# Optimization experiments

Hardware: AMD Instinct MI355X
Metric: run time of the kernel (lower is better)

## Reference

```python
import jax, jax.numpy as jnp
import numpy as np

B, S, D, H, F = 64, 512, 1024, 1024, 1024  # note: module requires H == D
EPS = 1e-6


def setup_inputs() -> dict:
    key = jax.random.key(0)
    ks = jax.random.split(key, 14)
    p = lambda k, shape: 0.02 * jax.random.normal(k, shape, dtype=jnp.float32)
    return {
        "hidden_state": jax.random.normal(ks[0], (B, S, D), dtype=jnp.float32),
        "field_hidden_state": jax.random.normal(ks[1], (B, S, F), dtype=jnp.float32),
        "input": jax.random.normal(ks[2], (B, D), dtype=jnp.float32),
        "finished": jnp.zeros((B, 1), dtype=bool),
        "W1": p(ks[3], (H, D)), "b1": p(ks[4], (H,)),
        "W2": p(ks[5], (H, D)), "b2": p(ks[6], (H,)),
        "W3": p(ks[7], (H, 2 * D)), "b3": p(ks[8], (H,)),
        "W4": p(ks[9], (H, F)), "b4": p(ks[10], (H,)),
        "W5": p(ks[11], (H, D)), "b5": p(ks[12], (H,)),
    }


def _norm_over_seq(w):
    # manual exp/max/sum softmax over seq dim (axis 0) with 1e-6 guard, as in torch
    w = jnp.exp(w - jnp.max(w, axis=0, keepdims=True))
    return w / (EPS + jnp.sum(w, axis=0, keepdims=True))


def reference(hidden_state, field_hidden_state, input, finished,
              W1, b1, W2, b2, W3, b3, W4, b4, W5, b5):
    hs = jnp.transpose(hidden_state, (1, 0, 2))        # [S, B, D]
    fs = jnp.transpose(field_hidden_state, (1, 0, 2))  # [S, B, F]
    phi_h = jnp.tanh(hs @ W1.T + b1)                   # [S, B, H]
    phi_f = jnp.tanh(fs @ W4.T + b4)                   # [S, B, H]

    gamma_h = jnp.tanh(input @ W2.T + b2)              # [B, H]
    weights = _norm_over_seq(jnp.sum(phi_h * gamma_h, axis=2, keepdims=True))  # [S, B, 1]

    alpha_h = jnp.tanh(input @ W5.T + b5)              # [B, H]
    field_w = _norm_over_seq(jnp.sum(phi_f * alpha_h, axis=2, keepdims=True))  # [S, B, 1]

    wf = weights * field_w
    weights = wf / (EPS + jnp.sum(wf, axis=0, keepdims=True))  # [S, B, 1]

    context = jnp.sum(hs * weights, axis=0)            # [B, D]
    out = jnp.concatenate([context, input], axis=-1) @ W3.T + b3  # [B, H]
    out = jnp.where(finished, jnp.zeros_like(out), out)
    return out, weights
```

## Files before the change

kernel.cpp:

```cpp
#include <hip/hip_runtime.h>

#define EPS 1e-6f

typedef _Float16 f16;
typedef __fp16 h16x2 __attribute__((ext_vector_type(2)));
typedef _Float16 f16x4 __attribute__((ext_vector_type(4)));
typedef _Float16 f16x8 __attribute__((ext_vector_type(8)));
typedef float f32x4 __attribute__((ext_vector_type(4)));

__device__ __forceinline__ float tanh_fast(float x) {
    float e = __expf(2.0f * x);
    return 1.0f - 2.0f / (e + 1.0f);
}

__global__ __launch_bounds__(256) void wconv_kernel(
    const float* __restrict__ W1, const float* __restrict__ W4,
    f16* __restrict__ W1h, f16* __restrict__ W4h)
{
    int gid = blockIdx.x * 256 + threadIdx.x;
    const float4* s1 = (const float4*)W1;
    const float4* s4 = (const float4*)W4;
    f16x4* d1 = (f16x4*)W1h;
    f16x4* d4 = (f16x4*)W4h;
    #pragma unroll
    for (int r = 0; r < 2; ++r) {
        int i = gid + r * 131072;
        float4 v = s1[i];
        f16x4 o; o[0]=(f16)v.x; o[1]=(f16)v.y; o[2]=(f16)v.z; o[3]=(f16)v.w;
        d1[i] = o;
        float4 u = s4[i];
        f16x4 p; p[0]=(f16)u.x; p[1]=(f16)u.y; p[2]=(f16)u.z; p[3]=(f16)u.w;
        d4[i] = p;
    }
}

__global__ __launch_bounds__(256) void gamal_kernel(
    const float* __restrict__ inp,
    const float* __restrict__ W2, const float* __restrict__ b2,
    const float* __restrict__ W5, const float* __restrict__ b5,
    float* __restrict__ gamm, float* __restrict__ alph)
{
    const float* W  = blockIdx.y ? W5 : W2;
    const float* bs = blockIdx.y ? b5 : b2;
    float* dst      = blockIdx.y ? alph : gamm;
    int wid = threadIdx.x >> 6, lane = threadIdx.x & 63;
    int p = blockIdx.x * 4 + wid;
    int b = p >> 10, h = p & 1023;
    const float4* wr = (const float4*)(W + (size_t)h * 1024);
    const float4* xr = (const float4*)(inp + (size_t)b * 1024);
    float acc = 0.f;
    #pragma unroll
    for (int j = 0; j < 4; ++j) {
        float4 w4 = wr[lane + 64 * j];
        float4 x4 = xr[lane + 64 * j];
        acc += w4.x * x4.x + w4.y * x4.y + w4.z * x4.z + w4.w * x4.w;
    }
    #pragma unroll
    for (int o = 32; o; o >>= 1) acc += __shfl_xor(acc, o);
    if (lane == 0) dst[p] = tanh_fast(acc + bs[h]);
}

__global__ __launch_bounds__(512, 1) void gemm_logits_kernel(
    const float* __restrict__ Ahid, const float* __restrict__ Afld,
    const f16* __restrict__ W1h, const f16* __restrict__ W4h,
    const float* __restrict__ b1, const float* __restrict__ b4,
    const float* __restrict__ gamm, const float* __restrict__ alph,
    float* __restrict__ Lpart)
{
    __shared__ __align__(16) char smA[2][32768];
    __shared__ __align__(16) char smW[2][32768];
    __shared__ float rowpart[256][4];

    const int lin = blockIdx.x;
    const int swz = (lin & 7) * 128 + (lin >> 3);
    const int mat = swz >> 9;
    const int rem = swz & 511;
    const int m_blk = rem >> 2;
    const int nc = rem & 3;
    const int m0 = m_blk << 8;
    const int hc0 = nc << 8;

    const float* A  = mat ? Afld : Ahid;
    const f16*  W   = mat ? W4h : W1h;
    const float* bv = mat ? b4 : b1;
    const float* gv = mat ? alph : gamm;

    const int t = threadIdx.x;
    const int lane = t & 63;
    const int wv = t >> 6;
    const int wr = wv >> 2;
    const int wc = wv & 3;
    const int c16 = lane & 15;
    const int kg = lane >> 4;

    const int srow = t >> 1;
    const int shalf = t & 1;
    const float* aRow = A + (size_t)(m0 + srow) * 1024 + shalf * 32;

    const int lrow = lane >> 3, lslot = lane & 7;
    const int kchunk = lslot ^ lrow;

    const int swzr = (c16 & 7) << 4;
    const int aoffb = (wr * 128 + c16) * 128;
    const int woffb = (wc * 64 + c16) * 128;
    const int kg16 = kg * 16;

    f32x4 acc[8][4];
    #pragma unroll
    for (int i = 0; i < 8; ++i)
        #pragma unroll
        for (int j = 0; j < 4; ++j) acc[i][j] = (f32x4){0.f, 0.f, 0.f, 0.f};

    float4 a_ld[8];

    auto loadA = [&](int kt) {
        const float4* ap = (const float4*)(aRow + kt * 64);
        #pragma unroll
        for (int j = 0; j < 8; ++j) a_ld[j] = ap[j];
    };
    auto writeA = [&](char* buf) {
        char* ad = buf + srow * 128;
        const int swzw = (srow & 7) << 4;
        const int wb = shalf * 64;
        #pragma unroll
        for (int j = 0; j < 4; ++j) {
            union { f16x8 v; h16x2 h[4]; } u;
            float4 x = a_ld[2 * j], y = a_ld[2 * j + 1];
            u.h[0] = __builtin_amdgcn_cvt_pkrtz(x.x, x.y);
            u.h[1] = __builtin_amdgcn_cvt_pkrtz(x.z, x.w);
            u.h[2] = __builtin_amdgcn_cvt_pkrtz(y.x, y.y);
            u.h[3] = __builtin_amdgcn_cvt_pkrtz(y.z, y.w);
            *(f16x8*)(ad + ((wb + j * 16) ^ swzw)) = u.v;
        }
    };
    auto gloadW = [&](int kt, char* buf) {
        #pragma unroll
        for (int j = 0; j < 4; ++j) {
            int r = wv * 32 + j * 8;
            const f16* src = W + (size_t)(hc0 + r + lrow) * 1024 + kt * 64 + kchunk * 8;
            char* dst = buf + r * 128;
            __builtin_amdgcn_global_load_lds(
                (const __attribute__((address_space(1))) void*)src,
                (__attribute__((address_space(3))) void*)dst, 16, 0, 0);
        }
    };

    loadA(0);
    gloadW(0, smW[0]);
    writeA(smA[0]);
    loadA(1);
    asm volatile("s_waitcnt vmcnt(8) lgkmcnt(0)" ::: "memory");
    __builtin_amdgcn_sched_barrier(0);
    __builtin_amdgcn_s_barrier();
    __builtin_amdgcn_sched_barrier(0);

    int cur = 0;
    for (int kt = 0; kt < 16; ++kt) {
        const int ktn  = kt < 15 ? kt + 1 : 15;
        const int ktnn = kt < 14 ? kt + 2 : 15;
        char* aC = smA[cur];
        char* wC = smW[cur];
        char* aN = smA[cur ^ 1];
        char* wN = smW[cur ^ 1];

        gloadW(ktn, wN);

        {
            f16x8 af[8], wf[4];
            const int ko = kg16 ^ swzr;
            #pragma unroll
            for (int mi = 0; mi < 8; ++mi) af[mi] = *(const f16x8*)(aC + aoffb + mi * 2048 + ko);
            #pragma unroll
            for (int ni = 0; ni < 4; ++ni) wf[ni] = *(const f16x8*)(wC + woffb + ni * 2048 + ko);
            __builtin_amdgcn_s_setprio(1);
            #pragma unroll
            for (int ni = 0; ni < 4; ++ni)
                #pragma unroll
                for (int mi = 0; mi < 8; ++mi)
                    acc[mi][ni] = __builtin_amdgcn_mfma_f32_16x16x32_f16(af[mi], wf[ni], acc[mi][ni], 0, 0, 0);
            __builtin_amdgcn_s_setprio(0);
        }

        writeA(aN);
        loadA(ktnn);
        __builtin_amdgcn_sched_barrier(0);

        {
            f16x8 af[8], wf[4];
            const int ko = (64 + kg16) ^ swzr;
            #pragma unroll
            for (int mi = 0; mi < 8; ++mi) af[mi] = *(const f16x8*)(aC + aoffb + mi * 2048 + ko);
            #pragma unroll
            for (int ni = 0; ni < 4; ++ni) wf[ni] = *(const f16x8*)(wC + woffb + ni * 2048 + ko);
            __builtin_amdgcn_s_setprio(1);
            #pragma unroll
            for (int ni = 0; ni < 4; ++ni)
                #pragma unroll
                for (int mi = 0; mi < 8; ++mi)
                    acc[mi][ni] = __builtin_amdgcn_mfma_f32_16x16x32_f16(af[mi], wf[ni], acc[mi][ni], 0, 0, 0);
            __builtin_amdgcn_s_setprio(0);
        }

        asm volatile("s_waitcnt vmcnt(8) lgkmcnt(0)" ::: "memory");
        __builtin_amdgcn_sched_barrier(0);
        __builtin_amdgcn_s_barrier();
        __builtin_amdgcn_sched_barrier(0);
        cur ^= 1;
    }

    const int bidx = m_blk >> 1;
    float g[4], bb[4];
    #pragma unroll
    for (int ni = 0; ni < 4; ++ni) {
        int h = hc0 + wc * 64 + ni * 16 + c16;
        g[ni]  = gv[(bidx << 10) + h];
        bb[ni] = bv[h];
    }
    #pragma unroll
    for (int mi = 0; mi < 8; ++mi) {
        #pragma unroll
        for (int q = 0; q < 4; ++q) {
            float v = tanh_fast(acc[mi][0][q] + bb[0]) * g[0]
                    + tanh_fast(acc[mi][1][q] + bb[1]) * g[1]
                    + tanh_fast(acc[mi][2][q] + bb[2]) * g[2]
                    + tanh_fast(acc[mi][3][q] + bb[3]) * g[3];
            v += __shfl_xor(v, 1);
            v += __shfl_xor(v, 2);
            v += __shfl_xor(v, 4);
            v += __shfl_xor(v, 8);
            if (c16 == 0)
                rowpart[wr * 128 + mi * 16 + kg * 4 + q][wc] = v;
        }
    }
    __syncthreads();
    if (t < 256)
        Lpart[(size_t)(mat * 4 + nc) * 32768 + m0 + t] =
            rowpart[t][0] + rowpart[t][1] + rowpart[t][2] + rowpart[t][3];
}

__device__ __forceinline__ float blockMax(float v, float* sm) {
    #pragma unroll
    for (int o = 32; o; o >>= 1) v = fmaxf(v, __shfl_xor(v, o));
    if ((threadIdx.x & 63) == 0) sm[threadIdx.x >> 6] = v;
    __syncthreads();
    v = fmaxf(fmaxf(sm[0], sm[1]), fmaxf(sm[2], sm[3]));
    __syncthreads();
    return v;
}
__device__ __forceinline__ float blockSum(float v, float* sm) {
    #pragma unroll
    for (int o = 32; o; o >>= 1) v += __shfl_xor(v, o);
    if ((threadIdx.x & 63) == 0) sm[threadIdx.x >> 6] = v;
    __syncthreads();
    v = sm[0] + sm[1] + sm[2] + sm[3];
    __syncthreads();
    return v;
}

__global__ __launch_bounds__(256) void softmax_combine_kernel(
    const float* __restrict__ Lp,
    float* __restrict__ wfin, float* __restrict__ dout)
{
    __shared__ float sm[4];
    int b = blockIdx.x, t = threadIdx.x;
    float h0 = 0.f, h1 = 0.f, f0 = 0.f, f1 = 0.f;
    #pragma unroll
    for (int nc = 0; nc < 4; ++nc) {
        h0 += Lp[nc * 32768 + b * 512 + t];
        h1 += Lp[nc * 32768 + b * 512 + 256 + t];
        f0 += Lp[(4 + nc) * 32768 + b * 512 + t];
        f1 += Lp[(4 + nc) * 32768 + b * 512 + 256 + t];
    }
    float mh = blockMax(fmaxf(h0, h1), sm);
    float mf = blockMax(fmaxf(f0, f1), sm);
    float e0 = __expf(h0 - mh), e1 = __expf(h1 - mh);
    float q0 = __expf(f0 - mf), q1 = __expf(f1 - mf);
    float sh = blockSum(e0 + e1, sm);
    float sf = blockSum(q0 + q1, sm);
    float wh0 = e0 / (EPS + sh), wh1 = e1 / (EPS + sh);
    float wq0 = q0 / (EPS + sf), wq1 = q1 / (EPS + sf);
    float c0 = wh0 * wq0, c1 = wh1 * wq1;
    float sc = blockSum(c0 + c1, sm);
    float r0 = c0 / (EPS + sc), r1 = c1 / (EPS + sc);
    wfin[b * 512 + t]       = r0;
    wfin[b * 512 + 256 + t] = r1;
    dout[65536 + t * 64 + b]         = r0;
    dout[65536 + (256 + t) * 64 + b] = r1;
}

__global__ __launch_bounds__(256) void context_kernel(
    const float* __restrict__ hs, const float* __restrict__ wgt,
    float* __restrict__ ctxpart)
{
    int dq = blockIdx.x;
    int b  = blockIdx.y;
    int sh = blockIdx.z;
    int t = threadIdx.x;
    int ss = t >> 6, ds = t & 63;
    __shared__ float4 part[4][64];
    const float4* hp = (const float4*)hs;
    float ax = 0.f, ay = 0.f, az = 0.f, aw = 0.f;
    int sBase = sh * 256 + ss * 64;
    for (int i = 0; i < 64; ++i) {
        int s = sBase + i;
        float w = wgt[b * 512 + s];
        float4 v = hp[(size_t)(b * 512 + s) * 256 + dq * 64 + ds];
        ax += v.x * w; ay += v.y * w; az += v.z * w; aw += v.w * w;
    }
    float4 r; r.x = ax; r.y = ay; r.z = az; r.w = aw;
    part[ss][ds] = r;
    __syncthreads();
    if (ss == 0) {
        float4 a0 = part[0][ds], a1 = part[1][ds], a2 = part[2][ds], a3 = part[3][ds];
        float4 o;
        o.x = a0.x + a1.x + a2.x + a3.x;
        o.y = a0.y + a1.y + a2.y + a3.y;
        o.z = a0.z + a1.z + a2.z + a3.z;
        o.w = a0.w + a1.w + a2.w + a3.w;
        ((float4*)ctxpart)[(size_t)sh * 16384 + b * 256 + dq * 64 + ds] = o;
    }
}

__global__ __launch_bounds__(256) void out_kernel(
    const float* __restrict__ ctxpart, const float* __restrict__ inp,
    const float* __restrict__ W3, const float* __restrict__ b3,
    const unsigned char* __restrict__ fin, float* __restrict__ out)
{
    int t = threadIdx.x, wid = t >> 6, lane = t & 63;
    int h = blockIdx.x * 4 + wid;
    __shared__ __align__(16) float xs[2048];
    float4* xsv = (float4*)xs;
    float4 wreg[8];
    const float4* w3r = (const float4*)(W3 + (size_t)h * 2048);
    #pragma unroll
    for (int j = 0; j < 8; ++j) wreg[j] = w3r[lane + 64 * j];
    const float4* cp = (const float4*)ctxpart;
    const float4* xp = (const float4*)inp;
    for (int b = 0; b < 64; ++b) {
        __syncthreads();
        {
            float4 c0 = cp[b * 256 + t];
            float4 c1 = cp[16384 + b * 256 + t];
            float4 cc; cc.x = c0.x + c1.x; cc.y = c0.y + c1.y;
            cc.z = c0.z + c1.z; cc.w = c0.w + c1.w;
            xsv[t] = cc;
            xsv[256 + t] = xp[b * 256 + t];
        }
        __syncthreads();
        float acc = 0.f;
        #pragma unroll
        for (int j = 0; j < 8; ++j) {
            float4 x = xsv[lane + 64 * j];
            acc += wreg[j].x * x.x + wreg[j].y * x.y + wreg[j].z * x.z + wreg[j].w * x.w;
        }
        #pragma unroll
        for (int o = 32; o; o >>= 1) acc += __shfl_xor(acc, o);
        if (lane == 0) out[b * 1024 + h] = fin[b] ? 0.f : (acc + b3[h]);
    }
}

extern "C" void kernel_launch(void* const* d_in, const int* in_sizes, int n_in,
                              void* d_out, int out_size, void* d_ws, size_t ws_size,
                              hipStream_t stream)
{
    const float* hidden = (const float*)d_in[0];
    const float* field  = (const float*)d_in[1];
    const float* input  = (const float*)d_in[2];
    const unsigned char* fin = (const unsigned char*)d_in[3];
    const float* W1 = (const float*)d_in[4];
    const float* b1 = (const float*)d_in[5];
    const float* W2 = (const float*)d_in[6];
    const float* b2 = (const float*)d_in[7];
    const float* W3 = (const float*)d_in[8];
    const float* b3 = (const float*)d_in[9];
    const float* W4 = (const float*)d_in[10];
    const float* b4 = (const float*)d_in[11];
    const float* W5 = (const float*)d_in[12];
    const float* b5 = (const float*)d_in[13];
    float* out = (float*)d_out;

    char* ws = (char*)d_ws;
    float* Lpart = (float*)(ws);
    float* wfin  = (float*)(ws + 1048576);
    float* gamm  = (float*)(ws + 1179648);
    float* alph  = (float*)(ws + 1441792);
    float* ctxp  = (float*)(ws + 1703936);
    f16*   W1h   = (f16*)(ws + 2228224);
    f16*   W4h   = (f16*)(ws + 4325376);

    wconv_kernel<<<512, 256, 0, stream>>>(W1, W4, W1h, W4h);
    gamal_kernel<<<dim3(16384, 2), 256, 0, stream>>>(input, W2, b2, W5, b5, gamm, alph);
    gemm_logits_kernel<<<1024, 512, 0, stream>>>(hidden, field, W1h, W4h,
                                                 b1, b4, gamm, alph, Lpart);
    softmax_combine_kernel<<<64, 256, 0, stream>>>(Lpart, wfin, out);
    context_kernel<<<dim3(4, 64, 2), 256, 0, stream>>>(hidden, wfin, ctxp);
    out_kernel<<<256, 256, 0, stream>>>(ctxp, input, W3, b3, fin, out);
}
```

Measured before the change: 379.4 us.

## Split GEMM k-step into four interleaved phases with staggered loads and barriers

Restructures the main GEMM loop so each k-tile is computed in four smaller MFMA clusters of 4x4 tiles instead of two 8x4 clusters. The W global-to-LDS loads and the A conversion writes are split into halves and interleaved between the clusters, with extra workgroup barriers intended to keep waves in lockstep so memory and matrix work overlap. This lowers register pressure for fragments but adds many more barriers and lgkmcnt waits per iteration, which can serialize the waves.

```diff
diff --git a/kernel.cpp b/kernel.cpp
--- a/kernel.cpp
+++ b/kernel.cpp
@@ -118,24 +118,24 @@
         #pragma unroll
         for (int j = 0; j < 8; ++j) a_ld[j] = ap[j];
     };
-    auto writeA = [&](char* buf) {
+    auto writeA_half = [&](char* buf, int h) {
         char* ad = buf + srow * 128;
         const int swzw = (srow & 7) << 4;
         const int wb = shalf * 64;
         #pragma unroll
-        for (int j = 0; j < 4; ++j) {
-            union { f16x8 v; h16x2 h[4]; } u;
+        for (int j = 2 * h; j < 2 * h + 2; ++j) {
+            union { f16x8 v; h16x2 q[4]; } u;
             float4 x = a_ld[2 * j], y = a_ld[2 * j + 1];
-            u.h[0] = __builtin_amdgcn_cvt_pkrtz(x.x, x.y);
-            u.h[1] = __builtin_amdgcn_cvt_pkrtz(x.z, x.w);
-            u.h[2] = __builtin_amdgcn_cvt_pkrtz(y.x, y.y);
-            u.h[3] = __builtin_amdgcn_cvt_pkrtz(y.z, y.w);
+            u.q[0] = __builtin_amdgcn_cvt_pkrtz(x.x, x.y);
+            u.q[1] = __builtin_amdgcn_cvt_pkrtz(x.z, x.w);
+            u.q[2] = __builtin_amdgcn_cvt_pkrtz(y.x, y.y);
+            u.q[3] = __builtin_amdgcn_cvt_pkrtz(y.z, y.w);
             *(f16x8*)(ad + ((wb + j * 16) ^ swzw)) = u.v;
         }
     };
-    auto gloadW = [&](int kt, char* buf) {
-        #pragma unroll
-        for (int j = 0; j < 4; ++j) {
+    auto gloadW_half = [&](int kt, char* buf, int h) {
+        #pragma unroll
+        for (int j = 2 * h; j < 2 * h + 2; ++j) {
             int r = wv * 32 + j * 8;
             const f16* src = W + (size_t)(hc0 + r + lrow) * 1024 + kt * 64 + kchunk * 8;
             char* dst = buf + r * 128;
@@ -146,13 +146,14 @@
     };
 
     loadA(0);
-    gloadW(0, smW[0]);
-    writeA(smA[0]);
+    gloadW_half(0, smW[0], 0);
+    gloadW_half(0, smW[0], 1);
+    writeA_half(smA[0], 0);
+    writeA_half(smA[0], 1);
     loadA(1);
     asm volatile("s_waitcnt vmcnt(8) lgkmcnt(0)" ::: "memory");
     __builtin_amdgcn_sched_barrier(0);
     __builtin_amdgcn_s_barrier();
-    __builtin_amdgcn_sched_barrier(0);
 
     int cur = 0;
     for (int kt = 0; kt < 16; ++kt) {
@@ -162,49 +163,77 @@
         char* wC = smW[cur];
         char* aN = smA[cur ^ 1];
         char* wN = smW[cur ^ 1];
-
-        gloadW(ktn, wN);
-
-        {
-            f16x8 af[8], wf[4];
-            const int ko = kg16 ^ swzr;
+        const int ko0 = kg16 ^ swzr;
+        const int ko1 = (64 + kg16) ^ swzr;
+
+        f16x8 af[4], wf[4];
+
+        #pragma unroll
+        for (int i = 0; i < 4; ++i) af[i] = *(const f16x8*)(aC + aoffb + i * 2048 + ko0);
+        #pragma unroll
+        for (int i = 0; i < 4; ++i) wf[i] = *(const f16x8*)(wC + woffb + i * 2048 + ko0);
+        gloadW_half(ktn, wN, 0);
+        __builtin_amdgcn_s_barrier();
+        asm volatile("s_waitcnt lgkmcnt(0)" ::: "memory");
+        __builtin_amdgcn_sched_barrier(0);
+        __builtin_amdgcn_s_setprio(1);
+        #pragma unroll
+        for (int ni = 0; ni < 4; ++ni)
             #pragma unroll
-            for (int mi = 0; mi < 8; ++mi) af[mi] = *(const f16x8*)(aC + aoffb + mi * 2048 + ko);
+            for (int mi = 0; mi < 4; ++mi)
+                acc[mi][ni] = __builtin_amdgcn_mfma_f32_16x16x32_f16(af[mi], wf[ni], acc[mi][ni], 0, 0, 0);
+        __builtin_amdgcn_s_setprio(0);
+        __builtin_amdgcn_s_barrier();
+
+        #pragma unroll
+        for (int i = 0; i < 4; ++i) af[i] = *(const f16x8*)(aC + aoffb + (i + 4) * 2048 + ko0);
+        gloadW_half(ktn, wN, 1);
+        writeA_half(aN, 0);
+        __builtin_amdgcn_s_barrier();
+        asm volatile("s_waitcnt lgkmcnt(0)" ::: "memory");
+        __builtin_amdgcn_sched_barrier(0);
+        __builtin_amdgcn_s_setprio(1);
+        #pragma unroll
+        for (int ni = 0; ni < 4; ++ni)
             #pragma unroll
-            for (int ni = 0; ni < 4; ++ni) wf[ni] = *(const f16x8*)(wC + woffb + ni * 2048 + ko);
-            __builtin_amdgcn_s_setprio(1);
+            for (int mi = 0; mi < 4; ++mi)
+                acc[mi + 4][ni] = __builtin_amdgcn_mfma_f32_16x16x32_f16(af[mi], wf[ni], acc[mi + 4][ni], 0, 0, 0);
+        __builtin_amdgcn_s_setprio(0);
+        __builtin_amdgcn_s_barrier();
+
+        #pragma unroll
+        for (int i = 0; i < 4; ++i) af[i] = *(const f16x8*)(aC + aoffb + i * 2048 + ko1);
+        #pragma unroll
+        for (int i = 0; i < 4; ++i) wf[i] = *(const f16x8*)(wC + woffb + i * 2048 + ko1);
+        writeA_half(aN, 1);
+        __builtin_amdgcn_s_barrier();
+        asm volatile("s_waitcnt lgkmcnt(0)" ::: "memory");
+        __builtin_amdgcn_sched_barrier(0);
+        __builtin_amdgcn_s_setprio(1);
+        #pragma unroll
+        for (int ni = 0; ni < 4; ++ni)
             #pragma unroll
-            for (int ni = 0; ni < 4; ++ni)
-                #pragma unroll
-                for (int mi = 0; mi < 8; ++mi)
-                    acc[mi][ni] = __builtin_amdgcn_mfma_f32_16x16x32_f16(af[mi], wf[ni], acc[mi][ni], 0, 0, 0);
-            __builtin_amdgcn_s_setprio(0);
-        }
-
-        writeA(aN);
+            for (int mi = 0; mi < 4; ++mi)
+                acc[mi][ni] = __builtin_amdgcn_mfma_f32_16x16x32_f16(af[mi], wf[ni], acc[mi][ni], 0, 0, 0);
+        __builtin_amdgcn_s_setprio(0);
+        __builtin_amdgcn_s_barrier();
+
+        #pragma unroll
+        for (int i = 0; i < 4; ++i) af[i] = *(const f16x8*)(aC + aoffb + (i + 4) * 2048 + ko1);
         loadA(ktnn);
+        __builtin_amdgcn_s_barrier();
+        asm volatile("s_waitcnt lgkmcnt(0)" ::: "memory");
         __builtin_amdgcn_sched_barrier(0);
-
-        {
-            f16x8 af[8], wf[4];
-            const int ko = (64 + kg16) ^ swzr;
+        __builtin_amdgcn_s_setprio(1);
+        #pragma unroll
+        for (int ni = 0; ni < 4; ++ni)
             #pragma unroll
-            for (int mi = 0; mi < 8; ++mi) af[mi] = *(const f16x8*)(aC + aoffb + mi * 2048 + ko);
-            #pragma unroll
-            for (int ni = 0; ni < 4; ++ni) wf[ni] = *(const f16x8*)(wC + woffb + ni * 2048 + ko);
-            __builtin_amdgcn_s_setprio(1);
-            #pragma unroll
-            for (int ni = 0; ni < 4; ++ni)
-                #pragma unroll
-                for (int mi = 0; mi < 8; ++mi)
-                    acc[mi][ni] = __builtin_amdgcn_mfma_f32_16x16x32_f16(af[mi], wf[ni], acc[mi][ni], 0, 0, 0);
-            __builtin_amdgcn_s_setprio(0);
-        }
-
-        asm volatile("s_waitcnt vmcnt(8) lgkmcnt(0)" ::: "memory");
+            for (int mi = 0; mi < 4; ++mi)
+                acc[mi + 4][ni] = __builtin_amdgcn_mfma_f32_16x16x32_f16(af[mi], wf[ni], acc[mi + 4][ni], 0, 0, 0);
+        __builtin_amdgcn_s_setprio(0);
+        asm volatile("s_waitcnt vmcnt(8)" ::: "memory");
         __builtin_amdgcn_sched_barrier(0);
         __builtin_amdgcn_s_barrier();
-        __builtin_amdgcn_sched_barrier(0);
         cur ^= 1;
     }
 
```

Result: slower. 419.3 us (+10.5%).
